# Optimization experiments

Hardware: AMD Instinct MI355X
Metric: run time of the kernel (lower is better)

Reference implementation:

```python
import jax, jax.numpy as jnp
import numpy as np

B, S, D_IN, D_E = 8, 2048, 1024, 1024


def setup_inputs() -> dict:
    key = jax.random.key(0)
    ks = jax.random.split(key, 9)
    s_in = 1.0 / np.sqrt(D_IN)
    s_e = 1.0 / np.sqrt(D_E)
    return {
        "x": jax.random.normal(ks[0], (B, S, D_IN), dtype=jnp.float32),
        "Wq": jax.random.uniform(ks[1], (D_IN, D_E), jnp.float32, -s_in, s_in),
        "bq": jax.random.uniform(ks[2], (D_E,), jnp.float32, -s_in, s_in),
        "Wk": jax.random.uniform(ks[3], (D_IN, D_E), jnp.float32, -s_in, s_in),
        "bk": jax.random.uniform(ks[4], (D_E,), jnp.float32, -s_in, s_in),
        "Wv": jax.random.uniform(ks[5], (D_IN, D_E), jnp.float32, -s_in, s_in),
        "bv": jax.random.uniform(ks[6], (D_E,), jnp.float32, -s_in, s_in),
        "Wo": jax.random.uniform(ks[7], (D_E, D_E), jnp.float32, -s_e, s_e),
        "bo": jax.random.uniform(ks[8], (D_E,), jnp.float32, -s_e, s_e),
    }


def reference(x, Wq, bq, Wk, bk, Wv, bv, Wo, bo):
    # QKV projections: [B,S,D_in] @ [D_in,D_e] -> [B,S,D_e]
    Q = jnp.einsum("bsi,ie->bse", x, Wq) + bq
    K = jnp.einsum("bsi,ie->bse", x, Wk) + bk
    V = jnp.einsum("bsi,ie->bse", x, Wv) + bv
    scale = 1.0 / jnp.sqrt(jnp.asarray(Q.shape[-1], Q.dtype))
    # full score matrix [B,S,S] (faithful to the unfused original)
    logits = jnp.einsum("bqe,bke->bqk", Q, K) * scale
    attn = jax.nn.softmax(logits, axis=-1)
    values = jnp.einsum("bqk,bke->bqe", attn, V)
    o = jnp.einsum("bqe,ef->bqf", values, Wo) + bo
    return o
```

## Files before the change

### kernel.cpp

```cpp
#include <hip/hip_runtime.h>

#define DIN 1024
#define DE  1024
#define SEQ 2048
#define NB  8

typedef __bf16 bf16x8 __attribute__((ext_vector_type(8)));
typedef float  f32x4  __attribute__((ext_vector_type(4)));
typedef unsigned short u16;
typedef u16 u16x8 __attribute__((ext_vector_type(8)));
typedef u16 u16x4 __attribute__((ext_vector_type(4)));

__device__ __forceinline__ u16 f2bf(float f) {
  unsigned u = __builtin_bit_cast(unsigned, f);
  return (u16)((u + 0x7FFFu + ((u >> 16) & 1u)) >> 16);
}
__device__ __forceinline__ float bf2f(u16 h) {
  return __builtin_bit_cast(float, (unsigned)h << 16);
}

typedef __attribute__((address_space(1))) const unsigned char g_u8;
typedef __attribute__((address_space(3))) unsigned char l_u8;
__device__ __forceinline__ void gload16(const void* g, void* l) {
  __builtin_amdgcn_global_load_lds((g_u8*)g, (l_u8*)l, 16, 0, 0);
}

__global__ __launch_bounds__(256) void cvt_f32_bf16(const float* __restrict__ in,
                                                    u16* __restrict__ out, int n4) {
  int i = blockIdx.x * 256 + threadIdx.x;
  if (i >= n4) return;
  float4 v = ((const float4*)in)[i];
  u16x4 o;
  o[0] = f2bf(v.x); o[1] = f2bf(v.y); o[2] = f2bf(v.z); o[3] = f2bf(v.w);
  ((u16x4*)out)[i] = o;
}

__global__ __launch_bounds__(256) void transpose_w(const float* __restrict__ W,
                                                   u16* __restrict__ Wt) {
  __shared__ float t[32][33];
  const int tx = threadIdx.x, ty = threadIdx.y;
  const int bx = blockIdx.x * 32, by = blockIdx.y * 32;
#pragma unroll
  for (int i = 0; i < 4; ++i)
    t[ty + i * 8][tx] = W[(size_t)(by + ty + i * 8) * 1024 + bx + tx];
  __syncthreads();
#pragma unroll
  for (int i = 0; i < 4; ++i)
    Wt[(size_t)(bx + ty + i * 8) * 1024 + by + tx] = f2bf(t[tx][ty + i * 8]);
}

__global__ __launch_bounds__(256) void softmax_rows_bf16(u16* __restrict__ P) {
  const size_t row = blockIdx.x;
  u16* pr = P + row * 2048 + (size_t)threadIdx.x * 8;
  u16x8 v = *(const u16x8*)pr;
  float x[8];
#pragma unroll
  for (int j = 0; j < 8; ++j) x[j] = bf2f(v[j]);
  float m = x[0];
#pragma unroll
  for (int j = 1; j < 8; ++j) m = fmaxf(m, x[j]);
#pragma unroll
  for (int off = 32; off; off >>= 1) m = fmaxf(m, __shfl_xor(m, off));
  __shared__ float rm[4], rs[4];
  const int lane = threadIdx.x & 63, wid = threadIdx.x >> 6;
  if (lane == 0) rm[wid] = m;
  __syncthreads();
  m = fmaxf(fmaxf(rm[0], rm[1]), fmaxf(rm[2], rm[3]));
  float s = 0.f;
#pragma unroll
  for (int j = 0; j < 8; ++j) { x[j] = __expf(x[j] - m); s += x[j]; }
#pragma unroll
  for (int off = 32; off; off >>= 1) s += __shfl_xor(s, off);
  if (lane == 0) rs[wid] = s;
  __syncthreads();
  s = (rs[0] + rs[1]) + (rs[2] + rs[3]);
  const float inv = 1.f / s;
  u16x8 o;
#pragma unroll
  for (int j = 0; j < 8; ++j) o[j] = f2bf(x[j] * inv);
  *(u16x8*)pr = o;
}

#define READF(BUFI, AV, BV)                                                   \
  {                                                                           \
    const char* _b = lds + (BUFI) * 32768;                                    \
    _Pragma("unroll") for (int n_ = 0; n_ < 4; ++n_)                          \
        BV[n_] = *(const bf16x8*)(_b + boffB + n_ * 1024);                    \
    _Pragma("unroll") for (int m_ = 0; m_ < 8; ++m_)                          \
        AV[m_] = *(const bf16x8*)(_b + aoffB + m_ * 1024);                    \
  }
#define MFMAF(AV, BV)                                                         \
  {                                                                           \
    __builtin_amdgcn_s_setprio(1);                                            \
    _Pragma("unroll") for (int m_ = 0; m_ < 8; ++m_)                          \
        _Pragma("unroll") for (int n_ = 0; n_ < 4; ++n_)                      \
            acc[m_][n_] = __builtin_amdgcn_mfma_f32_16x16x32_bf16(            \
                AV[m_], BV[n_], acc[m_][n_], 0, 0, 0);                        \
    __builtin_amdgcn_s_setprio(0);                                            \
  }

template <int OMODE, bool HAS_BIAS>
__global__ __launch_bounds__(512, 2) void gemmrp(
    const u16* __restrict__ A, const u16* __restrict__ Bt, void* __restrict__ C0,
    u16* __restrict__ C1, u16* __restrict__ C2, const float* __restrict__ b0,
    const float* __restrict__ b1, const float* __restrict__ b2,
    int M, int Nout, int K, size_t sA, size_t sB, size_t sC, float scale) {
  __shared__ __align__(16) char lds[4 * 32768];
  const int tid = threadIdx.x, lane = tid & 63, wid = tid >> 6;
  const int wm = wid >> 2, wn = wid & 3;
  const int lane15 = lane & 15, gk = lane >> 4;

  const int gx = gridDim.x, gy = gridDim.y;
  int lin = blockIdx.x + gx * (blockIdx.y + gy * blockIdx.z);
  const int nwg = gx * gy * (int)gridDim.z;
  const int q = nwg >> 3, r8 = nwg & 7;
  const int xcd = lin & 7, idx = lin >> 3;
  lin = (xcd < r8 ? xcd * (q + 1) : r8 * (q + 1) + (xcd - r8) * q) + idx;
  const int bz = lin / (gx * gy);
  const int rem = lin - bz * (gx * gy);
  const int by = rem / gx, bx = rem - (rem / gx) * gx;

  const char* Ag = (const char*)(A + (size_t)bz * sA + (size_t)by * 256 * K);
  const char* Bg = (const char*)(Bt + (size_t)bz * sB + (size_t)bx * 256 * K);
  const size_t Kb = (size_t)K * 2;

  const char* sa[2];
  const char* sb[2];
  int dA[2], dB[2];
#pragma unroll
  for (int j = 0; j < 2; ++j) {
    const int ls = j * 512 + tid, pr = ls >> 2, ps = ls & 3;
    const int g = ps ^ ((pr >> 1) & 3);
    sa[j] = Ag + (size_t)pr * Kb + g * 16;
    sb[j] = Bg + (size_t)pr * Kb + g * 16;
    dA[j] = ls * 16;
    dB[j] = 16384 + ls * 16;
  }
  auto stage = [&](int b) {
    char* base = lds + b * 32768;
#pragma unroll
    for (int j = 0; j < 2; ++j) {
      gload16(sa[j], base + dA[j]);
      gload16(sb[j], base + dB[j]);
      sa[j] += 64; sb[j] += 64;
    }
  };

  const int sw = (gk ^ ((lane15 >> 1) & 3)) << 4;
  const int aoffB = wm * 8192 + lane15 * 64 + sw;
  const int boffB = 16384 + wn * 4096 + lane15 * 64 + sw;

  f32x4 acc[8][4] = {};
  bf16x8 pa[8], pb[4], qa[8], qb[4];
  const int NT = K >> 5;

  stage(0); stage(1); stage(2);
  asm volatile("s_waitcnt vmcnt(4)" ::: "memory");
  __builtin_amdgcn_s_barrier();
  __builtin_amdgcn_sched_barrier(0);
  READF(0, pa, pb);

  for (int t = 0; t < NT; t += 2) {
    if (t + 3 < NT) stage((t + 3) & 3);
    READF((t + 1) & 3, qa, qb);
    __builtin_amdgcn_sched_barrier(0);
    MFMAF(pa, pb);
    if (t + 3 < NT) asm volatile("s_waitcnt vmcnt(4)" ::: "memory");
    else            asm volatile("s_waitcnt vmcnt(0)" ::: "memory");
    __builtin_amdgcn_s_barrier();
    __builtin_amdgcn_sched_barrier(0);
    if (t + 4 < NT) stage((t + 4) & 3);
    if (t + 2 < NT) READF((t + 2) & 3, pa, pb);
    __builtin_amdgcn_sched_barrier(0);
    MFMAF(qa, qb);
    if (t + 4 < NT) asm volatile("s_waitcnt vmcnt(4)" ::: "memory");
    else            asm volatile("s_waitcnt vmcnt(0)" ::: "memory");
    __builtin_amdgcn_s_barrier();
    __builtin_amdgcn_sched_barrier(0);
  }

  const int rbase = by * 256 + wm * 128 + (gk << 2);
  const int cbase = bx * 256 + wn * 64 + lane15;
#pragma unroll
  for (int m = 0; m < 8; ++m)
#pragma unroll
    for (int n = 0; n < 4; ++n) {
      const int col = cbase + n * 16;
      if (OMODE == 3) {
        u16* Cp; int ccol; const float* bp;
        if (col < 1024)      { Cp = (u16*)C0; ccol = col;        bp = b0; }
        else if (col < 2048) { Cp = C1;       ccol = col - 1024; bp = b1; }
        else                 { Cp = C2;       ccol = col - 2048; bp = b2; }
        const float bval = bp[ccol];
#pragma unroll
        for (int r = 0; r < 4; ++r) {
          const int rowg = rbase + m * 16 + r;
          const float v = acc[m][n][r] + bval;
          if (col < 2048)
            Cp[(size_t)rowg * 1024 + ccol] = f2bf(v);
          else
            Cp[(size_t)(rowg >> 11) * ((size_t)DE * SEQ) +
               (size_t)ccol * SEQ + (rowg & 2047)] = f2bf(v);
        }
      } else {
        const float bval = HAS_BIAS ? b0[col] : 0.f;
#pragma unroll
        for (int r = 0; r < 4; ++r) {
          const int rowg = rbase + m * 16 + r;
          const float v = acc[m][n][r] * scale + bval;
          if (OMODE == 0)
            ((float*)C0)[(size_t)bz * sC + (size_t)rowg * Nout + col] = v;
          else
            ((u16*)C0)[(size_t)bz * sC + (size_t)rowg * Nout + col] = f2bf(v);
        }
      }
    }
}

extern "C" void kernel_launch(void* const* d_in, const int* in_sizes, int n_in,
                              void* d_out, int out_size, void* d_ws, size_t ws_size,
                              hipStream_t stream) {
  const float* x  = (const float*)d_in[0];
  const float* Wq = (const float*)d_in[1];
  const float* bq = (const float*)d_in[2];
  const float* Wk = (const float*)d_in[3];
  const float* bk = (const float*)d_in[4];
  const float* Wv = (const float*)d_in[5];
  const float* bv = (const float*)d_in[6];
  const float* Wo = (const float*)d_in[7];
  const float* bo = (const float*)d_in[8];

  const size_t NEED = 142606336;
  if (ws_size < NEED) return;
  char* ws = (char*)d_ws;
  u16* x_bf = (u16*)(ws);
  u16* q_bf = (u16*)(ws + 33554432);
  u16* k_bf = (u16*)(ws + 67108864);
  u16* vt   = (u16*)(ws + 100663296);
  u16* wt   = (u16*)(ws + 134217728);
  u16* lgP  = (u16*)d_out;
  u16* wt_q = wt;
  u16* wt_k = wt + 1048576;
  u16* wt_v = wt + 2097152;
  u16* wt_o = wt + 3145728;

  dim3 tb(32, 8);
  const size_t sQ = (size_t)SEQ * DE;
  const size_t sL = (size_t)SEQ * SEQ;

  cvt_f32_bf16<<<16384, 256, 0, stream>>>(x, x_bf, (NB * SEQ * DIN) / 4);
  transpose_w<<<dim3(32, 32), tb, 0, stream>>>(Wq, wt_q);
  transpose_w<<<dim3(32, 32), tb, 0, stream>>>(Wk, wt_k);
  transpose_w<<<dim3(32, 32), tb, 0, stream>>>(Wv, wt_v);
  transpose_w<<<dim3(32, 32), tb, 0, stream>>>(Wo, wt_o);
  gemmrp<3, true><<<dim3(12, 64, 1), 512, 0, stream>>>(x_bf, wt, q_bf, k_bf, vt,
      bq, bk, bv, 16384, 1024, 1024, 0, 0, 0, 1.f);
  gemmrp<1, false><<<dim3(8, 8, 8), 512, 0, stream>>>(q_bf, k_bf, lgP,
      nullptr, nullptr, nullptr, nullptr, nullptr,
      2048, 2048, 1024, sQ, sQ, sL, 0.03125f);
  softmax_rows_bf16<<<16384, 256, 0, stream>>>(lgP);
  gemmrp<1, false><<<dim3(4, 8, 8), 512, 0, stream>>>(lgP, vt, q_bf,
      nullptr, nullptr, nullptr, nullptr, nullptr,
      2048, 1024, 2048, sL, sQ, sQ, 1.f);
  gemmrp<0, true><<<dim3(4, 64, 1), 512, 0, stream>>>(q_bf, wt_o, d_out,
      nullptr, nullptr, bo, nullptr, nullptr,
      16384, 1024, 1024, 0, 0, 0, 1.f);

  (void)in_sizes; (void)n_in; (void)out_size; (void)ws_size;
}
```

Measured before the change: 388.4 us.

## Restructure GEMM main loop to split-prefetch half of A fragments

Rewrites the GEMM K-loop so each step loads only the B fragments and the second half of the A fragments from the current LDS buffer. The first half of A for the next step is prefetched into a ping-pong register set. This cuts the register footprint of double-buffered fragments (from 24 to 16 bf16x8 vectors) and spreads LDS reads across MFMA phases. It also drops the minimum-blocks-per-CU hint from launch bounds, which changes the compiler's register budget and may lower occupancy.

```diff
diff --git a/kernel.cpp b/kernel.cpp
--- a/kernel.cpp
+++ b/kernel.cpp
@@ -81,26 +81,39 @@
   *(u16x8*)pr = o;
 }
 
-#define READF(BUFI, AV, BV)                                                   \
-  {                                                                           \
-    const char* _b = lds + (BUFI) * 32768;                                    \
-    _Pragma("unroll") for (int n_ = 0; n_ < 4; ++n_)                          \
-        BV[n_] = *(const bf16x8*)(_b + boffB + n_ * 1024);                    \
-    _Pragma("unroll") for (int m_ = 0; m_ < 8; ++m_)                          \
-        AV[m_] = *(const bf16x8*)(_b + aoffB + m_ * 1024);                    \
+#define BODYT(T, AP, AN)                                                       \
+  {                                                                            \
+    const int t_ = (T);                                                        \
+    if (t_ + 3 < NT) stage((t_ + 3) & 3);                                      \
+    const char* cb_ = lds + (t_ & 3) * 32768;                                  \
+    const char* nb_ = lds + ((t_ + 1) & 3) * 32768;                            \
+    _Pragma("unroll") for (int n_ = 0; n_ < 4; ++n_)                           \
+        bv[n_] = *(const bf16x8*)(cb_ + boffB + n_ * 1024);                    \
+    _Pragma("unroll") for (int m_ = 0; m_ < 4; ++m_)                           \
+        aF[m_] = *(const bf16x8*)(cb_ + aoffB + (4 + m_) * 1024);              \
+    if (t_ + 1 < NT) {                                                         \
+      _Pragma("unroll") for (int m_ = 0; m_ < 4; ++m_)                         \
+          AN[m_] = *(const bf16x8*)(nb_ + aoffB + m_ * 1024);                  \
+    }                                                                          \
+    __builtin_amdgcn_sched_barrier(0);                                         \
+    __builtin_amdgcn_s_setprio(1);                                             \
+    _Pragma("unroll") for (int m_ = 0; m_ < 4; ++m_)                           \
+        _Pragma("unroll") for (int n_ = 0; n_ < 4; ++n_)                       \
+            acc[m_][n_] = __builtin_amdgcn_mfma_f32_16x16x32_bf16(             \
+                AP[m_], bv[n_], acc[m_][n_], 0, 0, 0);                         \
+    _Pragma("unroll") for (int m_ = 0; m_ < 4; ++m_)                           \
+        _Pragma("unroll") for (int n_ = 0; n_ < 4; ++n_)                       \
+            acc[4 + m_][n_] = __builtin_amdgcn_mfma_f32_16x16x32_bf16(         \
+                aF[m_], bv[n_], acc[4 + m_][n_], 0, 0, 0);                     \
+    __builtin_amdgcn_s_setprio(0);                                             \
+    if (t_ + 3 < NT) asm volatile("s_waitcnt vmcnt(4)" ::: "memory");          \
+    else             asm volatile("s_waitcnt vmcnt(0)" ::: "memory");          \
+    __builtin_amdgcn_s_barrier();                                              \
+    __builtin_amdgcn_sched_barrier(0);                                         \
   }
-#define MFMAF(AV, BV)                                                         \
-  {                                                                           \
-    __builtin_amdgcn_s_setprio(1);                                            \
-    _Pragma("unroll") for (int m_ = 0; m_ < 8; ++m_)                          \
-        _Pragma("unroll") for (int n_ = 0; n_ < 4; ++n_)                      \
-            acc[m_][n_] = __builtin_amdgcn_mfma_f32_16x16x32_bf16(            \
-                AV[m_], BV[n_], acc[m_][n_], 0, 0, 0);                        \
-    __builtin_amdgcn_s_setprio(0);                                            \
-  }
 
 template <int OMODE, bool HAS_BIAS>
-__global__ __launch_bounds__(512, 2) void gemmrp(
+__global__ __launch_bounds__(512) void gemmpl(
     const u16* __restrict__ A, const u16* __restrict__ Bt, void* __restrict__ C0,
     u16* __restrict__ C1, u16* __restrict__ C2, const float* __restrict__ b0,
     const float* __restrict__ b1, const float* __restrict__ b2,
@@ -151,32 +164,19 @@
   const int boffB = 16384 + wn * 4096 + lane15 * 64 + sw;
 
   f32x4 acc[8][4] = {};
-  bf16x8 pa[8], pb[4], qa[8], qb[4];
+  bf16x8 aA[4], aB[4], aF[4], bv[4];
   const int NT = K >> 5;
 
   stage(0); stage(1); stage(2);
   asm volatile("s_waitcnt vmcnt(4)" ::: "memory");
   __builtin_amdgcn_s_barrier();
   __builtin_amdgcn_sched_barrier(0);
-  READF(0, pa, pb);
+#pragma unroll
+  for (int m = 0; m < 4; ++m) aA[m] = *(const bf16x8*)(lds + aoffB + m * 1024);
 
   for (int t = 0; t < NT; t += 2) {
-    if (t + 3 < NT) stage((t + 3) & 3);
-    READF((t + 1) & 3, qa, qb);
-    __builtin_amdgcn_sched_barrier(0);
-    MFMAF(pa, pb);
-    if (t + 3 < NT) asm volatile("s_waitcnt vmcnt(4)" ::: "memory");
-    else            asm volatile("s_waitcnt vmcnt(0)" ::: "memory");
-    __builtin_amdgcn_s_barrier();
-    __builtin_amdgcn_sched_barrier(0);
-    if (t + 4 < NT) stage((t + 4) & 3);
-    if (t + 2 < NT) READF((t + 2) & 3, pa, pb);
-    __builtin_amdgcn_sched_barrier(0);
-    MFMAF(qa, qb);
-    if (t + 4 < NT) asm volatile("s_waitcnt vmcnt(4)" ::: "memory");
-    else            asm volatile("s_waitcnt vmcnt(0)" ::: "memory");
-    __builtin_amdgcn_s_barrier();
-    __builtin_amdgcn_sched_barrier(0);
+    BODYT(t, aA, aB);
+    BODYT(t + 1, aB, aA);
   }
 
   const int rbase = by * 256 + wm * 128 + (gk << 2);
@@ -253,16 +253,16 @@
   transpose_w<<<dim3(32, 32), tb, 0, stream>>>(Wk, wt_k);
   transpose_w<<<dim3(32, 32), tb, 0, stream>>>(Wv, wt_v);
   transpose_w<<<dim3(32, 32), tb, 0, stream>>>(Wo, wt_o);
-  gemmrp<3, true><<<dim3(12, 64, 1), 512, 0, stream>>>(x_bf, wt, q_bf, k_bf, vt,
+  gemmpl<3, true><<<dim3(12, 64, 1), 512, 0, stream>>>(x_bf, wt, q_bf, k_bf, vt,
       bq, bk, bv, 16384, 1024, 1024, 0, 0, 0, 1.f);
-  gemmrp<1, false><<<dim3(8, 8, 8), 512, 0, stream>>>(q_bf, k_bf, lgP,
+  gemmpl<1, false><<<dim3(8, 8, 8), 512, 0, stream>>>(q_bf, k_bf, lgP,
       nullptr, nullptr, nullptr, nullptr, nullptr,
       2048, 2048, 1024, sQ, sQ, sL, 0.03125f);
   softmax_rows_bf16<<<16384, 256, 0, stream>>>(lgP);
-  gemmrp<1, false><<<dim3(4, 8, 8), 512, 0, stream>>>(lgP, vt, q_bf,
+  gemmpl<1, false><<<dim3(4, 8, 8), 512, 0, stream>>>(lgP, vt, q_bf,
       nullptr, nullptr, nullptr, nullptr, nullptr,
       2048, 1024, 2048, sL, sQ, sQ, 1.f);
-  gemmrp<0, true><<<dim3(4, 64, 1), 512, 0, stream>>>(q_bf, wt_o, d_out,
+  gemmpl<0, true><<<dim3(4, 64, 1), 512, 0, stream>>>(q_bf, wt_o, d_out,
       nullptr, nullptr, bo, nullptr, nullptr,
       16384, 1024, 1024, 0, 0, 0, 1.f);
 
```

Result: no change. 391.5 us (+0.8%).
